# Performance work log

Measured on AMD Instinct MI355X. Metric: run time of the kernel, lower is better.

The kernel has to match this reference:

```python
import jax, jax.numpy as jnp
import numpy as np

N, R, E = 100000, 3, 500000
IN_F, HID_F, OUT_F = 128, 128, 32


def setup_inputs() -> dict:
    key = jax.random.key(0)
    ks = jax.random.split(key, 12)
    inp = {
        "x": jax.random.normal(ks[0], (N, IN_F), dtype=jnp.float32),
        "src": jax.random.randint(ks[1], (R, E), 0, N, dtype=jnp.int32),
        "dst": jax.random.randint(ks[2], (R, E), 0, N, dtype=jnp.int32),
        # per-relation weights for the 4 layers (Glorot-ish scale)
        "W0": jax.random.normal(ks[3], (R, IN_F, HID_F), dtype=jnp.float32) / np.sqrt(IN_F),
        "b0": jnp.zeros((R, HID_F), dtype=jnp.float32),
        "W1": jax.random.normal(ks[4], (R, HID_F, HID_F), dtype=jnp.float32) / np.sqrt(HID_F),
        "b1": jnp.zeros((R, HID_F), dtype=jnp.float32),
        "W2": jax.random.normal(ks[5], (R, HID_F, HID_F), dtype=jnp.float32) / np.sqrt(HID_F),
        "b2": jnp.zeros((R, HID_F), dtype=jnp.float32),
        "W3": jax.random.normal(ks[6], (R, HID_F, OUT_F), dtype=jnp.float32) / np.sqrt(HID_F),
        "b3": jnp.zeros((R, OUT_F), dtype=jnp.float32),
    }
    return inp


def _degree_norms(src, dst, n_nodes):
    # DGL GraphConv norm='both': clamp degree to >=1, use deg^-1/2
    ones = jnp.ones(src.shape[1], dtype=jnp.float32)
    dout = jax.vmap(lambda s: jax.ops.segment_sum(ones, s, num_segments=n_nodes))(src)
    din = jax.vmap(lambda d: jax.ops.segment_sum(ones, d, num_segments=n_nodes))(dst)
    return jnp.clip(dout, 1.0) ** -0.5, jnp.clip(din, 1.0) ** -0.5  # [R, N] each


def _hetero_layer(h, W, b, src, dst, dout_is, din_is, relu):
    # per-relation GraphConv (norm='both'), HeteroGraphConv aggregate='sum'
    n = h.shape[0]
    out = None
    for r in range(W.shape[0]):
        hs = h * dout_is[r][:, None]                          # [N, d] scale src
        msg = hs[src[r]]                                       # [E, d] gather
        agg = jax.ops.segment_sum(msg, dst[r], num_segments=n) # [N, d] scatter-add
        agg = agg * din_is[r][:, None]
        o = agg @ W[r] + b[r]
        if relu:
            o = jax.nn.relu(o)  # activation inside GraphConv, before cross-rel sum
        out = o if out is None else out + o
    return out


def reference(x, src, dst, W0, b0, W1, b1, W2, b2, W3, b3):
    dout_is, din_is = _degree_norms(src, dst, x.shape[0])
    h = _hetero_layer(x, W0, b0, src, dst, dout_is, din_is, relu=True)
    h = _hetero_layer(h, W1, b1, src, dst, dout_is, din_is, relu=True)
    h = _hetero_layer(h, W2, b2, src, dst, dout_is, din_is, relu=True)
    h = _hetero_layer(h, W3, b3, src, dst, dout_is, din_is, relu=False)
    return h  # [N, OUT_F]
```

## Files before the change

kernel.cpp:

```cpp
#include <hip/hip_runtime.h>
#include <cstdint>
#include <cstddef>

#define NN 100000
#define RR 3
#define EE 500000
#define RN 300000
#define RE 1500000
#define CAP 32

typedef unsigned short u16;
typedef unsigned int   u32;
typedef __attribute__((ext_vector_type(8))) short bhalf8;
typedef __attribute__((ext_vector_type(4))) float f32x4;

static inline int cdiv_h(int a, int b){ return (a+b-1)/b; }

__device__ __forceinline__ float bf_lo(u32 v){ union{u32 u; float f;} c; c.u = v<<16; return c.f; }
__device__ __forceinline__ float bf_hi(u32 v){ union{u32 u; float f;} c; c.u = v & 0xffff0000u; return c.f; }
__device__ __forceinline__ u16 f2bf(float f){
  union{float f; u32 u;} c; c.f = f;
  u32 r = (c.u + 0x7FFFu + ((c.u >> 16) & 1u)) >> 16;
  return (u16)r;
}
__device__ __forceinline__ u32 pk2(float a, float b){ return (u32)f2bf(a) | ((u32)f2bf(b)<<16); }

__global__ __launch_bounds__(256) void k_init(int* __restrict__ cursor, int* __restrict__ dout_cnt){
  int i = blockIdx.x*256 + threadIdx.x;
  if (i < RN){ cursor[i] = i*CAP; dout_cnt[i] = 0; }
}

__global__ __launch_bounds__(256) void k_pre1f(const int* __restrict__ src, const int* __restrict__ dst,
    int* __restrict__ cursor, int* __restrict__ dout_cnt, int* __restrict__ edge_src,
    const float* __restrict__ x, u16* __restrict__ xb,
    const float* __restrict__ W0, const float* __restrict__ W1, const float* __restrict__ W2,
    const float* __restrict__ W3, u16* __restrict__ Wtb, u16* __restrict__ Wt3b){
  int b = blockIdx.x, t = threadIdx.x;
  if (b < 5860){
    int i = b*256 + t;
    if (i < RE){
      int r = i / EE;
      int s = src[i], d = dst[i];
      atomicAdd(&dout_cnt[r*NN + s], 1);
      int idx = r*NN + d;
      int pos = atomicAdd(&cursor[idx], 1);
      if (pos < idx*CAP + CAP) edge_src[pos] = s;
    }
  } else if (b < 12110){
    int i = (b-5860)*256 + t;
    if (i < NN*128/8){
      float4 v0 = ((const float4*)x)[i*2];
      float4 v1 = ((const float4*)x)[i*2+1];
      uint4 o;
      o.x = pk2(v0.x, v0.y); o.y = pk2(v0.z, v0.w);
      o.z = pk2(v1.x, v1.y); o.w = pk2(v1.z, v1.w);
      ((uint4*)xb)[i] = o;
    }
  } else if (b < 12686){
    int gid = (b-12110)*256 + t;
    if (gid < 3*3*16384){
      int l = gid / 49152; int rem = gid - l*49152;
      int r = rem >> 14; int rem2 = rem & 16383;
      int k = rem2 >> 7; int n = rem2 & 127;
      const float* Wl = (l==0) ? W0 : (l==1) ? W1 : W2;
      Wtb[((size_t)(l*3+r))*16384 + (size_t)n*128 + k] = f2bf(Wl[rem]);
    }
  } else {
    int gid = (b-12686)*256 + t;
    if (gid < 3*4096){
      int r = gid >> 12; int rem = gid & 4095;
      int k = rem >> 5; int n = rem & 31;
      Wt3b[(size_t)(r*32+n)*128 + k] = f2bf(W3[gid]);
    }
  }
}

__global__ __launch_bounds__(256) void k_norms(const int* __restrict__ dout_cnt, float* __restrict__ dout_is){
  int i = blockIdx.x*256 + threadIdx.x;
  if (i < RN){
    int dc = dout_cnt[i] > 1 ? dout_cnt[i] : 1;
    dout_is[i] = rsqrtf((float)dc);
  }
}

__global__ __launch_bounds__(256) void k_layer(const u16* __restrict__ h, const u16* __restrict__ Wt,
    const float* __restrict__ bias, const int* __restrict__ cursor,
    const int* __restrict__ edge_src, const float* __restrict__ dout_is, u16* __restrict__ out){
  __shared__ __align__(16) u16 As[128*128];
  __shared__ __align__(16) u16 Bs[128*128];
  int t = threadIdx.x;
  int l = t & 63, w = t >> 6;
  int wr = w >> 1, wc = w & 1;
  int row0 = blockIdx.x * 128;
  int tr = t >> 4, tc = t & 15;
  int g = l >> 4, k = l & 15;

  const uint4* __restrict__ h4 = (const uint4*)h;

  f32x4 res[4][4];
  #pragma unroll
  for (int m=0;m<4;m++)
    #pragma unroll
    for (int n=0;n<4;n++) res[m][n] = (f32x4){0.f,0.f,0.f,0.f};

  for (int r=0; r<RR; r++){
    if (r > 0) __syncthreads();

    uint4 rb[8];
    #pragma unroll
    for (int it=0; it<8; ++it)
      rb[it] = *(const uint4*)&Wt[(size_t)r*16384 + (size_t)(it*16+tr)*128 + tc*8];

    const float* __restrict__ dis = dout_is + r*NN;

    #pragma unroll 2
    for (int qd=0; qd<8; ++qd){
      int nl = w*32 + qd*4 + g;
      int node = row0 + nl;
      float a[8] = {0.f,0.f,0.f,0.f,0.f,0.f,0.f,0.f};
      int cnt = 0;
      if (node < NN){
        int widx = r*NN + node;
        int base = widx*CAP;
        cnt = cursor[widx] - base;
        if (cnt > CAP) cnt = CAP;
        int e = 0;
        for (; e+2 <= cnt; e += 2){
          int sa = edge_src[base+e], sb = edge_src[base+e+1];
          float wa = dis[sa], wb = dis[sb];
          uint4 va = h4[(size_t)sa*16 + k];
          uint4 vb = h4[(size_t)sb*16 + k];
          a[0]+=wa*bf_lo(va.x); a[1]+=wa*bf_hi(va.x); a[2]+=wa*bf_lo(va.y); a[3]+=wa*bf_hi(va.y);
          a[4]+=wa*bf_lo(va.z); a[5]+=wa*bf_hi(va.z); a[6]+=wa*bf_lo(va.w); a[7]+=wa*bf_hi(va.w);
          a[0]+=wb*bf_lo(vb.x); a[1]+=wb*bf_hi(vb.x); a[2]+=wb*bf_lo(vb.y); a[3]+=wb*bf_hi(vb.y);
          a[4]+=wb*bf_lo(vb.z); a[5]+=wb*bf_hi(vb.z); a[6]+=wb*bf_lo(vb.w); a[7]+=wb*bf_hi(vb.w);
        }
        if (e < cnt){
          int s = edge_src[base+e];
          float wa = dis[s];
          uint4 v = h4[(size_t)s*16 + k];
          a[0]+=wa*bf_lo(v.x); a[1]+=wa*bf_hi(v.x); a[2]+=wa*bf_lo(v.y); a[3]+=wa*bf_hi(v.y);
          a[4]+=wa*bf_lo(v.z); a[5]+=wa*bf_hi(v.z); a[6]+=wa*bf_lo(v.w); a[7]+=wa*bf_hi(v.w);
        }
      }
      float di = rsqrtf((float)(cnt > 1 ? cnt : 1));
      uint4 o;
      o.x = pk2(a[0]*di, a[1]*di); o.y = pk2(a[2]*di, a[3]*di);
      o.z = pk2(a[4]*di, a[5]*di); o.w = pk2(a[6]*di, a[7]*di);
      *(uint4*)&As[nl*128 + ((k ^ (nl&7))*8)] = o;
    }

    #pragma unroll
    for (int it=0; it<8; ++it){
      int rho = it*16 + tr;
      *(uint4*)&Bs[rho*128 + ((tc ^ (tr&7))*8)] = rb[it];
    }
    __syncthreads();

    f32x4 acc[4][4];
    #pragma unroll
    for (int m=0;m<4;m++)
      #pragma unroll
      for (int n=0;n<4;n++) acc[m][n] = (f32x4){0.f,0.f,0.f,0.f};

    #pragma unroll
    for (int kk=0; kk<4; ++kk){
      bhalf8 af[4], bf[4];
      #pragma unroll
      for (int m=0;m<4;m++){
        int rho = wr*64 + m*16 + (l&15);
        int ch = (kk*4 + (l>>4)) ^ (l&7);
        af[m] = *(const bhalf8*)&As[rho*128 + ch*8];
      }
      #pragma unroll
      for (int n=0;n<4;n++){
        int rho = wc*64 + n*16 + (l&15);
        int ch = (kk*4 + (l>>4)) ^ (l&7);
        bf[n] = *(const bhalf8*)&Bs[rho*128 + ch*8];
      }
      #pragma unroll
      for (int m=0;m<4;m++)
        #pragma unroll
        for (int n=0;n<4;n++)
          acc[m][n] = __builtin_amdgcn_mfma_f32_16x16x32_bf16(af[m], bf[n], acc[m][n], 0, 0, 0);
    }

    #pragma unroll
    for (int n=0;n<4;n++){
      int col = wc*64 + n*16 + (l&15);
      float bb = bias[r*128 + col];
      #pragma unroll
      for (int m=0;m<4;m++)
        #pragma unroll
        for (int i=0;i<4;i++){
          float v = acc[m][n][i] + bb;
          res[m][n][i] += v > 0.f ? v : 0.f;
        }
    }
  }

  #pragma unroll
  for (int m=0;m<4;m++)
    #pragma unroll
    for (int i=0;i<4;i++){
      int grow = row0 + wr*64 + m*16 + (l>>4)*4 + i;
      if (grow < NN){
        #pragma unroll
        for (int n=0;n<4;n++)
          out[(size_t)grow*128 + wc*64 + n*16 + (l&15)] = f2bf(res[m][n][i]);
      }
    }
}

__global__ __launch_bounds__(256) void k_mm_y(const u16* __restrict__ A, const u16* __restrict__ Wt3,
    u16* __restrict__ y){
  __shared__ __align__(16) u16 As[128*128];
  __shared__ __align__(16) u16 Bs[96*128];
  int t = threadIdx.x;
  int l = t & 63, w = t >> 6;
  int wr = w & 1, wc = w >> 1;
  int row0 = blockIdx.x * 128;
  int tr = t >> 4, tc = t & 15;
  int swz = tr & 7;

  uint4 ra[8], rb[6];
  #pragma unroll
  for (int it=0; it<8; ++it){
    int grow = row0 + it*16 + tr;
    if (grow > NN-1) grow = NN-1;
    ra[it] = *(const uint4*)&A[(size_t)grow*128 + tc*8];
  }
  #pragma unroll
  for (int it=0; it<6; ++it)
    rb[it] = *(const uint4*)&Wt3[(size_t)(it*16 + tr)*128 + tc*8];
  #pragma unroll
  for (int it=0; it<8; ++it)
    *(uint4*)&As[(it*16+tr)*128 + ((tc ^ swz)*8)] = ra[it];
  #pragma unroll
  for (int it=0; it<6; ++it)
    *(uint4*)&Bs[(it*16+tr)*128 + ((tc ^ swz)*8)] = rb[it];
  __syncthreads();

  f32x4 acc[4][3];
  #pragma unroll
  for (int m=0;m<4;m++)
    #pragma unroll
    for (int n=0;n<3;n++) acc[m][n] = (f32x4){0.f,0.f,0.f,0.f};

  #pragma unroll
  for (int kk=0; kk<4; ++kk){
    bhalf8 af[4], bf[3];
    #pragma unroll
    for (int m=0;m<4;m++){
      int rho = wr*64 + m*16 + (l&15);
      int ch = (kk*4 + (l>>4)) ^ (l&7);
      af[m] = *(const bhalf8*)&As[rho*128 + ch*8];
    }
    #pragma unroll
    for (int n=0;n<3;n++){
      int rho = wc*48 + n*16 + (l&15);
      int ch = (kk*4 + (l>>4)) ^ (l&7);
      bf[n] = *(const bhalf8*)&Bs[rho*128 + ch*8];
    }
    #pragma unroll
    for (int m=0;m<4;m++)
      #pragma unroll
      for (int n=0;n<3;n++)
        acc[m][n] = __builtin_amdgcn_mfma_f32_16x16x32_bf16(af[m], bf[n], acc[m][n], 0, 0, 0);
  }

  #pragma unroll
  for (int m=0;m<4;m++)
    #pragma unroll
    for (int i=0;i<4;i++){
      int grow = row0 + wr*64 + m*16 + (l>>4)*4 + i;
      if (grow < NN){
        #pragma unroll
        for (int n=0;n<3;n++)
          y[(size_t)grow*96 + wc*48 + n*16 + (l&15)] = f2bf(acc[m][n][i]);
      }
    }
}

__global__ __launch_bounds__(256) void k_agg_out(const u16* __restrict__ y, float* __restrict__ out,
    const int* __restrict__ cursor, const int* __restrict__ edge_src,
    const float* __restrict__ dout_is, const float* __restrict__ b3){
  int n = (blockIdx.x*256 + threadIdx.x) >> 6;
  if (n >= NN) return;
  int l = threadIdx.x & 63;
  int g = l >> 3, k = l & 7;
  float res[4];
  #pragma unroll
  for (int i=0;i<4;i++) res[i] = b3[4*k+i] + b3[32+4*k+i] + b3[64+4*k+i];
  const uint2* __restrict__ y2 = (const uint2*)y;
  for (int r=0; r<RR; r++){
    int w = r*NN + n;
    int s0 = w*CAP;
    int s1 = cursor[w];
    if (s1 > s0 + CAP) s1 = s0 + CAP;
    const float* __restrict__ dis = dout_is + r*NN;
    float a[4] = {0.f,0.f,0.f,0.f};
    for (int p = s0 + g; p < s1; p += 8){
      int s = edge_src[p];
      float wg = dis[s];
      uint2 v = y2[(size_t)s*24 + r*8 + k];
      a[0] += wg*bf_lo(v.x); a[1] += wg*bf_hi(v.x);
      a[2] += wg*bf_lo(v.y); a[3] += wg*bf_hi(v.y);
    }
    #pragma unroll
    for (int i=0;i<4;i++){
      a[i] += __shfl_xor(a[i], 8);
      a[i] += __shfl_xor(a[i], 16);
      a[i] += __shfl_xor(a[i], 32);
    }
    int cnt = s1 - s0;
    float di = rsqrtf((float)(cnt>1?cnt:1));
    #pragma unroll
    for (int i=0;i<4;i++) res[i] += di*a[i];
  }
  if (g == 0)
    ((float4*)out)[(size_t)n*8 + k] = make_float4(res[0],res[1],res[2],res[3]);
}


extern "C" void kernel_launch(void* const* d_in, const int* in_sizes, int n_in,
                              void* d_out, int out_size, void* d_ws, size_t ws_size,
                              hipStream_t stream){
  const float* x   = (const float*)d_in[0];
  const int*   src = (const int*)d_in[1];
  const int*   dst = (const int*)d_in[2];
  const float* W0  = (const float*)d_in[3]; const float* b0 = (const float*)d_in[4];
  const float* W1  = (const float*)d_in[5]; const float* b1 = (const float*)d_in[6];
  const float* W2  = (const float*)d_in[7]; const float* b2 = (const float*)d_in[8];
  const float* W3  = (const float*)d_in[9]; const float* b3 = (const float*)d_in[10];
  float* out = (float*)d_out;

  char* p = (char*)d_ws;
  auto alloc = [&](size_t bytes)->char*{
    char* q = p; p += (bytes + 255) & ~(size_t)255; return q;
  };
  int*   cursor   = (int*)  alloc(RN*4);
  int*   dout_cnt = (int*)  alloc(RN*4);
  float* dout_is  = (float*)alloc(RN*4);
  u16*   Wtb      = (u16*)  alloc((size_t)3*3*16384*2);
  u16*   Wt3b     = (u16*)  alloc((size_t)3*32*128*2);
  u16*   y        = (u16*)  alloc((size_t)NN*96*2);
  u16*   bufA     = (u16*)  alloc((size_t)NN*128*2);
  u16*   bufB     = (u16*)  alloc((size_t)NN*128*2);
  int*   edge_src = (int*)  alloc((size_t)RN*CAP*4);

  k_init <<<cdiv_h(RN,256),256,0,stream>>>(cursor, dout_cnt);
  k_pre1f<<<12734,256,0,stream>>>(src, dst, cursor, dout_cnt, edge_src,
                                  x, bufB, W0,W1,W2,W3, Wtb, Wt3b);
  k_norms<<<cdiv_h(RN,256),256,0,stream>>>(dout_cnt, dout_is);

  int mm_blocks = cdiv_h(NN,128);
  k_layer<<<mm_blocks,256,0,stream>>>(bufB, Wtb,           b0, cursor, edge_src, dout_is, bufA);
  k_layer<<<mm_blocks,256,0,stream>>>(bufA, Wtb + 3*16384, b1, cursor, edge_src, dout_is, bufB);
  k_layer<<<mm_blocks,256,0,stream>>>(bufB, Wtb + 6*16384, b2, cursor, edge_src, dout_is, bufA);
  k_mm_y<<<mm_blocks,256,0,stream>>>(bufA, Wt3b, y);
  k_agg_out<<<cdiv_h(NN,4),256,0,stream>>>(y, out, cursor, edge_src, dout_is, b3);
}
```

Before: 808.8 us.

## Split fused gather-GEMM layer into wavefront-per-node aggregation and separate GEMM kernel

The fused layer kernel, which gathered neighbor features into shared memory and then ran MFMA GEMM, is split into two kernels. A new aggregation kernel gives one wavefront to each (relation, node) pair, spreads edges over four lane groups and reduces them with shuffles, then writes a bf16 [N, 3*128] buffer. A separate GEMM kernel loads that buffer into LDS and multiplies it by the per-relation weights. The aim is more parallelism and latency hiding for the irregular gather, away from the GEMM tile's occupancy limits. The cost is an extra round trip through global memory for the aggregated features, plus more kernel launches.

```diff
diff --git a/kernel.cpp b/kernel.cpp
--- a/kernel.cpp
+++ b/kernel.cpp
@@ -7,6 +7,7 @@
 #define EE 500000
 #define RN 300000
 #define RE 1500000
+#define KK 384
 #define CAP 32
 
 typedef unsigned short u16;
@@ -83,9 +84,49 @@
   }
 }
 
-__global__ __launch_bounds__(256) void k_layer(const u16* __restrict__ h, const u16* __restrict__ Wt,
-    const float* __restrict__ bias, const int* __restrict__ cursor,
-    const int* __restrict__ edge_src, const float* __restrict__ dout_is, u16* __restrict__ out){
+__global__ __launch_bounds__(256) void k_agg_bf(const u16* __restrict__ h, u16* __restrict__ AGG,
+    const int* __restrict__ cursor, const int* __restrict__ edge_src,
+    const float* __restrict__ dout_is){
+  int w = (blockIdx.x*256 + threadIdx.x) >> 6;
+  if (w >= RN) return;
+  int l = threadIdx.x & 63;
+  int q = l >> 4, k = l & 15;
+  int r = w / NN;
+  int n = w - r*NN;
+  int s0 = w*CAP;
+  int s1 = cursor[w];
+  if (s1 > s0 + CAP) s1 = s0 + CAP;
+  const float* __restrict__ dis = dout_is + r*NN;
+  const uint4* __restrict__ h4 = (const uint4*)h;
+  float a[8] = {0.f,0.f,0.f,0.f,0.f,0.f,0.f,0.f};
+  for (int p = s0 + q; p < s1; p += 4){
+    int s = edge_src[p];
+    float wg = dis[s];
+    uint4 v = h4[(size_t)s*16 + k];
+    a[0] += wg*bf_lo(v.x); a[1] += wg*bf_hi(v.x);
+    a[2] += wg*bf_lo(v.y); a[3] += wg*bf_hi(v.y);
+    a[4] += wg*bf_lo(v.z); a[5] += wg*bf_hi(v.z);
+    a[6] += wg*bf_lo(v.w); a[7] += wg*bf_hi(v.w);
+  }
+  #pragma unroll
+  for (int i=0;i<8;i++){
+    a[i] += __shfl_xor(a[i], 16);
+    a[i] += __shfl_xor(a[i], 32);
+  }
+  if (q == 0){
+    int cnt = s1 - s0;
+    float di = rsqrtf((float)(cnt > 1 ? cnt : 1));
+    uint4 o;
+    o.x = pk2(a[0]*di, a[1]*di);
+    o.y = pk2(a[2]*di, a[3]*di);
+    o.z = pk2(a[4]*di, a[5]*di);
+    o.w = pk2(a[6]*di, a[7]*di);
+    ((uint4*)AGG)[(size_t)n*48 + r*16 + k] = o;
+  }
+}
+
+__global__ __launch_bounds__(256) void k_mm_relu(const u16* __restrict__ A, const u16* __restrict__ Wt,
+    const float* __restrict__ bias, u16* __restrict__ out){
   __shared__ __align__(16) u16 As[128*128];
   __shared__ __align__(16) u16 Bs[128*128];
   int t = threadIdx.x;
@@ -93,9 +134,7 @@
   int wr = w >> 1, wc = w & 1;
   int row0 = blockIdx.x * 128;
   int tr = t >> 4, tc = t & 15;
-  int g = l >> 4, k = l & 15;
-
-  const uint4* __restrict__ h4 = (const uint4*)h;
+  int swz = tr & 7;
 
   f32x4 res[4][4];
   #pragma unroll
@@ -104,56 +143,21 @@
     for (int n=0;n<4;n++) res[m][n] = (f32x4){0.f,0.f,0.f,0.f};
 
   for (int r=0; r<RR; r++){
-    if (r > 0) __syncthreads();
-
-    uint4 rb[8];
-    #pragma unroll
-    for (int it=0; it<8; ++it)
-      rb[it] = *(const uint4*)&Wt[(size_t)r*16384 + (size_t)(it*16+tr)*128 + tc*8];
-
-    const float* __restrict__ dis = dout_is + r*NN;
-
-    #pragma unroll 2
-    for (int qd=0; qd<8; ++qd){
-      int nl = w*32 + qd*4 + g;
-      int node = row0 + nl;
-      float a[8] = {0.f,0.f,0.f,0.f,0.f,0.f,0.f,0.f};
-      int cnt = 0;
-      if (node < NN){
-        int widx = r*NN + node;
-        int base = widx*CAP;
-        cnt = cursor[widx] - base;
-        if (cnt > CAP) cnt = CAP;
-        int e = 0;
-        for (; e+2 <= cnt; e += 2){
-          int sa = edge_src[base+e], sb = edge_src[base+e+1];
-          float wa = dis[sa], wb = dis[sb];
-          uint4 va = h4[(size_t)sa*16 + k];
-          uint4 vb = h4[(size_t)sb*16 + k];
-          a[0]+=wa*bf_lo(va.x); a[1]+=wa*bf_hi(va.x); a[2]+=wa*bf_lo(va.y); a[3]+=wa*bf_hi(va.y);
-          a[4]+=wa*bf_lo(va.z); a[5]+=wa*bf_hi(va.z); a[6]+=wa*bf_lo(va.w); a[7]+=wa*bf_hi(va.w);
-          a[0]+=wb*bf_lo(vb.x); a[1]+=wb*bf_hi(vb.x); a[2]+=wb*bf_lo(vb.y); a[3]+=wb*bf_hi(vb.y);
-          a[4]+=wb*bf_lo(vb.z); a[5]+=wb*bf_hi(vb.z); a[6]+=wb*bf_lo(vb.w); a[7]+=wb*bf_hi(vb.w);
-        }
-        if (e < cnt){
-          int s = edge_src[base+e];
-          float wa = dis[s];
-          uint4 v = h4[(size_t)s*16 + k];
-          a[0]+=wa*bf_lo(v.x); a[1]+=wa*bf_hi(v.x); a[2]+=wa*bf_lo(v.y); a[3]+=wa*bf_hi(v.y);
-          a[4]+=wa*bf_lo(v.z); a[5]+=wa*bf_hi(v.z); a[6]+=wa*bf_lo(v.w); a[7]+=wa*bf_hi(v.w);
-        }
-      }
-      float di = rsqrtf((float)(cnt > 1 ? cnt : 1));
-      uint4 o;
-      o.x = pk2(a[0]*di, a[1]*di); o.y = pk2(a[2]*di, a[3]*di);
-      o.z = pk2(a[4]*di, a[5]*di); o.w = pk2(a[6]*di, a[7]*di);
-      *(uint4*)&As[nl*128 + ((k ^ (nl&7))*8)] = o;
-    }
-
+    uint4 ra[8], rb[8];
+    #pragma unroll
+    for (int it=0; it<8; ++it){
+      int grow = row0 + it*16 + tr;
+      if (grow > NN-1) grow = NN-1;
+      ra[it] = *(const uint4*)&A[(size_t)grow*KK + r*128 + tc*8];
+      rb[it] = *(const uint4*)&Wt[(size_t)r*16384 + (size_t)(it*16 + tr)*128 + tc*8];
+    }
+    __syncthreads();
     #pragma unroll
     for (int it=0; it<8; ++it){
       int rho = it*16 + tr;
-      *(uint4*)&Bs[rho*128 + ((tc ^ (tr&7))*8)] = rb[it];
+      int ch = (tc ^ swz) * 8;
+      *(uint4*)&As[rho*128 + ch] = ra[it];
+      *(uint4*)&Bs[rho*128 + ch] = rb[it];
     }
     __syncthreads();
 
@@ -344,20 +348,26 @@
   float* dout_is  = (float*)alloc(RN*4);
   u16*   Wtb      = (u16*)  alloc((size_t)3*3*16384*2);
   u16*   Wt3b     = (u16*)  alloc((size_t)3*32*128*2);
-  u16*   y        = (u16*)  alloc((size_t)NN*96*2);
+  u16*   AGG      = (u16*)  alloc((size_t)NN*KK*2);
   u16*   bufA     = (u16*)  alloc((size_t)NN*128*2);
   u16*   bufB     = (u16*)  alloc((size_t)NN*128*2);
   int*   edge_src = (int*)  alloc((size_t)RN*CAP*4);
+  u16*   y        = AGG;
 
   k_init <<<cdiv_h(RN,256),256,0,stream>>>(cursor, dout_cnt);
   k_pre1f<<<12734,256,0,stream>>>(src, dst, cursor, dout_cnt, edge_src,
                                   x, bufB, W0,W1,W2,W3, Wtb, Wt3b);
   k_norms<<<cdiv_h(RN,256),256,0,stream>>>(dout_cnt, dout_is);
 
-  int mm_blocks = cdiv_h(NN,128);
-  k_layer<<<mm_blocks,256,0,stream>>>(bufB, Wtb,           b0, cursor, edge_src, dout_is, bufA);
-  k_layer<<<mm_blocks,256,0,stream>>>(bufA, Wtb + 3*16384, b1, cursor, edge_src, dout_is, bufB);
-  k_layer<<<mm_blocks,256,0,stream>>>(bufB, Wtb + 6*16384, b2, cursor, edge_src, dout_is, bufA);
+  int agg_blocks = cdiv_h(RN,4);
+  int mm_blocks  = cdiv_h(NN,128);
+
+  k_agg_bf<<<agg_blocks,256,0,stream>>>(bufB, AGG, cursor, edge_src, dout_is);
+  k_mm_relu<<<mm_blocks,256,0,stream>>>(AGG, Wtb, b0, bufA);
+  k_agg_bf<<<agg_blocks,256,0,stream>>>(bufA, AGG, cursor, edge_src, dout_is);
+  k_mm_relu<<<mm_blocks,256,0,stream>>>(AGG, Wtb + 3*16384, b1, bufB);
+  k_agg_bf<<<agg_blocks,256,0,stream>>>(bufB, AGG, cursor, edge_src, dout_is);
+  k_mm_relu<<<mm_blocks,256,0,stream>>>(AGG, Wtb + 6*16384, b2, bufA);
   k_mm_y<<<mm_blocks,256,0,stream>>>(bufA, Wt3b, y);
   k_agg_out<<<cdiv_h(NN,4),256,0,stream>>>(y, out, cursor, edge_src, dout_is, b3);
 }
```

Measured after the change: 776.3 us. 1.04x faster.
